# Optimization experiments

Hardware: AMD Instinct MI355X
Metric: run time of the kernel (lower is better)

The kernel has to match this reference:

```python
import jax, jax.numpy as jnp
import numpy as np

D_MODEL = 1024
NUM_HEADS = 16
DEPTH = D_MODEL // NUM_HEADS
MAX_LEN = 5000


def _make_pe(d_model=D_MODEL, max_len=MAX_LEN):
    # Faithful to torch PositionalEncoding: pe shape [max_len, 1, d_model]
    position = np.arange(max_len, dtype=np.float32)[:, None]
    div_term = np.exp(np.arange(0, d_model, 2, dtype=np.float32) * (-np.log(10000.0) / d_model))
    pe = np.zeros((max_len, d_model), dtype=np.float32)
    pe[:, 0::2] = np.sin(position * div_term)
    pe[:, 1::2] = np.cos(position * div_term)
    return jnp.asarray(pe[:, None, :])  # [max_len, 1, d_model]


def setup_inputs() -> dict:
    key = jax.random.key(0)
    ks = jax.random.split(key, 11)
    B, S, D = 4, 2048, D_MODEL
    s = 1.0 / np.sqrt(D)
    inp = {
        "v": jax.random.normal(ks[0], (B, S, D), jnp.float32),
        "k": jax.random.normal(ks[1], (B, S, D), jnp.float32),
        "q": jax.random.normal(ks[2], (B, S, D), jnp.float32),
        "wq_w": jax.random.normal(ks[3], (D, D), jnp.float32) * s,
        "wq_b": jnp.zeros((D,), jnp.float32),
        "wk_w": jax.random.normal(ks[4], (D, D), jnp.float32) * s,
        "wk_b": jnp.zeros((D,), jnp.float32),
        "wv_w": jax.random.normal(ks[5], (D, D), jnp.float32) * s,
        "wv_b": jnp.zeros((D,), jnp.float32),
        "dense_w": jax.random.normal(ks[6], (D, D), jnp.float32) * s,
        "dense_b": jnp.zeros((D,), jnp.float32),
        "pe": _make_pe(),
    }
    return inp


def _split_heads(x, B):
    # [B, S, D] -> [B, H, S, depth]
    return x.reshape(B, -1, NUM_HEADS, DEPTH).transpose(0, 2, 1, 3)


def reference(v, k, q, wq_w, wq_b, wk_w, wk_b, wv_w, wv_b, dense_w, dense_b, pe):
    B = q.shape[0]
    # Faithful bug-reproduction: pe[:batch] has shape [B, 1, D], broadcast over seq.
    pe_b = pe[:B]  # [B, 1, D]
    q = q + pe_b
    k = k + pe_b
    v = v + pe_b
    # Linear layers (torch: x @ W.T + b)
    qh = _split_heads(q @ wq_w.T + wq_b, B)  # [B,H,Sq,d]
    kh = _split_heads(k @ wk_w.T + wk_b, B)  # [B,H,Sk,d]
    vh = _split_heads(v @ wv_w.T + wv_b, B)  # [B,H,Sk,d]
    scale = 1.0 / jnp.sqrt(jnp.float32(DEPTH))
    logits = jnp.einsum("bhqd,bhkd->bhqk", qh, kh) * scale
    attn = jax.nn.softmax(logits, axis=-1)
    out = jnp.einsum("bhqk,bhkd->bhqd", attn, vh)
    out = out.transpose(0, 2, 1, 3).reshape(B, -1, D_MODEL)
    return out @ dense_w.T + dense_b
```

## Files before the change

kernel.cpp:

```cpp
#include <hip/hip_runtime.h>
#include <hip/hip_bf16.h>

typedef short short8 __attribute__((ext_vector_type(8)));
typedef float f32x4 __attribute__((ext_vector_type(4)));
typedef float f32x16 __attribute__((ext_vector_type(16)));
typedef unsigned int uint4v __attribute__((ext_vector_type(4)));

#define MFMA16(a, b, c) __builtin_amdgcn_mfma_f32_16x16x32_bf16(a, b, c, 0, 0, 0)
#define MFMA32(a, b, c) __builtin_amdgcn_mfma_f32_32x32x16_bf16(a, b, c, 0, 0, 0)

typedef __attribute__((address_space(1))) const unsigned int gas_u32;
typedef __attribute__((address_space(3))) unsigned int las_u32;

__device__ inline void gll16(const void* g, void* l) {
    __builtin_amdgcn_global_load_lds((gas_u32*)g, (las_u32*)l, 16, 0, 0);
}

__device__ inline unsigned short f2bf(float f) {
    unsigned u = __builtin_bit_cast(unsigned, f);
    u += 0x7fff + ((u >> 16) & 1);
    return (unsigned short)(u >> 16);
}

__device__ inline unsigned pk_trunc(float a, float b) {
    unsigned ua = __builtin_bit_cast(unsigned, a);
    unsigned ub = __builtin_bit_cast(unsigned, b);
    return (ua >> 16) | (ub & 0xFFFF0000u);
}

__device__ inline float exp2_fast(float x) {
#if __has_builtin(__builtin_amdgcn_exp2f)
    return __builtin_amdgcn_exp2f(x);
#else
    float r; asm("v_exp_f32 %0, %1" : "=v"(r) : "v"(x)); return r;
#endif
}

__device__ inline void pl32_swap(unsigned &a, unsigned &b) {
    asm volatile("v_permlane32_swap_b32 %0, %1" : "+v"(a), "+v"(b));
}

__global__ void pe_cast3(const float* __restrict__ q, const float* __restrict__ k,
                         const float* __restrict__ v, const float* __restrict__ pe,
                         unsigned short* __restrict__ oq, unsigned short* __restrict__ ok,
                         unsigned short* __restrict__ ov) {
    const float* x = (blockIdx.y == 0) ? q : (blockIdx.y == 1) ? k : v;
    unsigned short* o = (blockIdx.y == 0) ? oq : (blockIdx.y == 1) ? ok : ov;
    int i = blockIdx.x * 256 + threadIdx.x;
    long e = (long)i * 4;
    int b = (int)(e >> 21);
    int d = (int)(e & 1023);
    float4 xv = reinterpret_cast<const float4*>(x)[i];
    float4 pv = *reinterpret_cast<const float4*>(pe + b * 1024 + d);
    ushort4 r;
    r.x = f2bf(xv.x + pv.x); r.y = f2bf(xv.y + pv.y);
    r.z = f2bf(xv.z + pv.z); r.w = f2bf(xv.w + pv.w);
    reinterpret_cast<ushort4*>(o)[i] = r;
}

__global__ void wcast4(const float* __restrict__ w0, const float* __restrict__ w1,
                       const float* __restrict__ w2, const float* __restrict__ w3,
                       unsigned short* __restrict__ o0) {
    const float* w = (blockIdx.y == 0) ? w0 : (blockIdx.y == 1) ? w1
                   : (blockIdx.y == 2) ? w2 : w3;
    unsigned short* o = o0 + (size_t)blockIdx.y * 1024 * 1024;
    int i = blockIdx.x * 256 + threadIdx.x;
    float4 xv = reinterpret_cast<const float4*>(w)[i];
    ushort4 r;
    r.x = f2bf(xv.x); r.y = f2bf(xv.y); r.z = f2bf(xv.z); r.w = f2bf(xv.w);
    reinterpret_cast<ushort4*>(o)[i] = r;
}

template <int MODE>
__global__ __launch_bounds__(256, 4) void gemm3(const unsigned short* __restrict__ A0,
                                                const unsigned short* __restrict__ W0,
                                                const float* __restrict__ bq,
                                                const float* __restrict__ bk,
                                                const float* __restrict__ bv,
                                                void* __restrict__ oq,
                                                void* __restrict__ ok,
                                                void* __restrict__ ov,
                                                float qscale) {
    const int NT = 32;
    __shared__ unsigned short lsA[2][128 * 32];
    __shared__ unsigned short lsB[2][128 * 32];

    int z = (MODE == 3) ? blockIdx.z : 0;
    const unsigned short* A = A0 + (size_t)z * 8192 * 1024;
    const unsigned short* W = W0 + (size_t)z * 1024 * 1024;
    const float* bias = (MODE == 3) ? ((z == 0) ? bq : (z == 1) ? bk : bv) : bq;
    float scale = (MODE == 3 && z == 0) ? qscale : 1.0f;

    int tid = threadIdx.x;
    int wave = tid >> 6, lane = tid & 63, lg = lane >> 4, l15 = lane & 15;
    int brow = blockIdx.x * 128;
    int bcol = blockIdx.y * 128;
    int wr = wave >> 1, wc = wave & 1;

    f32x4 zero4 = {0.f, 0.f, 0.f, 0.f};
    f32x4 acc[4][4];
#pragma unroll
    for (int m = 0; m < 4; ++m)
#pragma unroll
        for (int n = 0; n < 4; ++n) acc[m][n] = zero4;

#define STG(k0, bi) do {                                                        \
        _Pragma("unroll")                                                       \
        for (int j = 0; j < 2; ++j) {                                           \
            int c = j * 256 + wave * 64 + lane;                                 \
            gll16(A + ((long)(brow + (c >> 2)) * 1024 + (k0) + (c & 3) * 8),    \
                  (char*)lsA[bi] + (j * 256 + wave * 64) * 16);                 \
            gll16(W + ((long)(bcol + (c >> 2)) * 1024 + (k0) + (c & 3) * 8),    \
                  (char*)lsB[bi] + (j * 256 + wave * 64) * 16);                 \
        }                                                                       \
    } while (0)

    STG(0, 0);
    __syncthreads();

    int cur = 0;
    for (int t = 0; t < NT; ++t) {
        if (t < NT - 1) STG((t + 1) * 32, cur ^ 1);

        const char* KA = (const char*)lsA[cur];
        const char* KB = (const char*)lsB[cur];
        short8 af[4], bf_[4];
#pragma unroll
        for (int m = 0; m < 4; ++m) {
            int row = wr * 64 + m * 16 + l15;
            af[m] = *(const short8*)(KA + row * 64 + lg * 16);
        }
#pragma unroll
        for (int n = 0; n < 4; ++n) {
            int col = wc * 64 + n * 16 + l15;
            bf_[n] = *(const short8*)(KB + col * 64 + lg * 16);
        }
#pragma unroll
        for (int m = 0; m < 4; ++m)
#pragma unroll
            for (int n = 0; n < 4; ++n) acc[m][n] = MFMA16(af[m], bf_[n], acc[m][n]);

        __syncthreads();
        cur ^= 1;
    }
#undef STG

    void* out = (MODE == 3) ? ((z == 0) ? oq : (z == 1) ? ok : ov) : oq;
#pragma unroll
    for (int m = 0; m < 4; ++m)
#pragma unroll
        for (int n = 0; n < 4; ++n) {
            int col = bcol + wc * 64 + n * 16 + l15;
            float bv_ = bias[col];
#pragma unroll
            for (int r = 0; r < 4; ++r) {
                int row = brow + wr * 64 + m * 16 + lg * 4 + r;
                float v = (acc[m][n][r] + bv_) * scale;
                if (MODE == 1) {
                    ((float*)out)[(long)row * 1024 + col] = v;
                } else {
                    int b = row >> 11, s = row & 2047;
                    if (z < 2) {
                        int h = col >> 6, d = col & 63;
                        ((unsigned short*)out)[(((long)(b * 16 + h) * 2048 + s) * 64 + d)] = f2bf(v);
                    } else {
                        ((unsigned short*)out)[((long)(b * 1024 + col)) * 2048 + s] = f2bf(v);
                    }
                }
            }
        }
}

__global__ __launch_bounds__(256, 2) void attn_kernel(const unsigned short* __restrict__ Qh,
                                                      const unsigned short* __restrict__ Kh,
                                                      const unsigned short* __restrict__ Vt,
                                                      unsigned short* __restrict__ Om) {
    const int S = 2048;
    const int NT = S / 64;
    int flat = blockIdx.x;
    int nf_ = (flat & 7) * 64 + (flat >> 3);
    int qt = nf_ & 7;
    int bh = nf_ >> 3;
    int b = bh >> 4, h = bh & 15;

    int tid = threadIdx.x, wave = tid >> 6, lane = tid & 63;
    int l31 = lane & 31, hi = lane >> 5;

    __shared__ __align__(16) unsigned short Kl[3][4096];
    __shared__ __align__(16) unsigned short Vtl[3][4096];

    const unsigned short* Qb = Qh + (long)bh * S * 64;
    const unsigned short* Kb = Kh + (long)bh * S * 64;
    const unsigned short* Vb = Vt + (long)bh * 64 * S;

    int colS = ((((tid & 7) * 16) ^ (((tid >> 3) & 7) << 4)) >> 1);
    const unsigned short* srcK = Kb + (tid >> 3) * 64 + colS;
    const unsigned short* srcV = Vb + (tid >> 3) * 2048 + colS;

    short8 aq[2][4];
    {
        const unsigned short* qrow = Qb + (long)(qt * 256 + wave * 64 + l31) * 64 + hi * 8;
#pragma unroll
        for (int qf = 0; qf < 2; ++qf)
#pragma unroll
            for (int s = 0; s < 4; ++s)
                aq[qf][s] = *(const short8*)(qrow + qf * 32 * 64 + s * 16);
    }

    f32x16 oacc[2][2], lacc[2];
#pragma unroll
    for (int r = 0; r < 16; ++r) {
        oacc[0][0][r] = 0.f; oacc[0][1][r] = 0.f;
        oacc[1][0][r] = 0.f; oacc[1][1][r] = 0.f;
        lacc[0][r] = 0.f; lacc[1][r] = 0.f;
    }

    const short8 ones8 = {0x3F80, 0x3F80, 0x3F80, 0x3F80, 0x3F80, 0x3F80, 0x3F80, 0x3F80};

    int rb0 = l31 * 128;
    int swz = (l31 & 7) << 4;

#define STAGE(kt, bi) do {                                              \
        const unsigned short* sk = srcK + (kt) * 4096;                  \
        gll16(sk,         (char*)Kl[bi] + wave * 1024);                 \
        gll16(sk + 2048,  (char*)Kl[bi] + 4096 + wave * 1024);          \
        const unsigned short* sv = srcV + (kt) * 64;                    \
        gll16(sv,         (char*)Vtl[bi] + wave * 1024);                \
        gll16(sv + 65536, (char*)Vtl[bi] + 4096 + wave * 1024);         \
    } while (0)

    STAGE(0, 0);
    STAGE(1, 1);

    int bi = 0, sb = 2;
    for (int kt = 0; kt < NT; ++kt) {
        if (kt == NT - 1) { asm volatile("s_waitcnt vmcnt(0)" ::: "memory"); }
        else              { asm volatile("s_waitcnt vmcnt(4)" ::: "memory"); }
        __builtin_amdgcn_s_barrier();
        if (kt < NT - 2) STAGE(kt + 2, sb);

        const char* KlC = (const char*)Kl[bi];
        const char* VlC = (const char*)Vtl[bi];

        f32x16 sacc[2][2];
#pragma unroll
        for (int r = 0; r < 16; ++r) {
            sacc[0][0][r] = 0.f; sacc[0][1][r] = 0.f;
            sacc[1][0][r] = 0.f; sacc[1][1][r] = 0.f;
        }
#pragma unroll
        for (int blk = 0; blk < 2; ++blk)
#pragma unroll
            for (int s = 0; s < 4; ++s) {
                short8 kf = *(const short8*)(KlC + blk * 4096 + rb0 + ((32 * s + 16 * hi) ^ swz));
                sacc[0][blk] = MFMA32(kf, aq[0][s], sacc[0][blk]);
                sacc[1][blk] = MFMA32(kf, aq[1][s], sacc[1][blk]);
            }

#pragma unroll
        for (int qf = 0; qf < 2; ++qf)
#pragma unroll
            for (int blk = 0; blk < 2; ++blk)
#pragma unroll
                for (int r = 0; r < 16; ++r) sacc[qf][blk][r] = exp2_fast(sacc[qf][blk][r]);

#pragma unroll
        for (int s = 0; s < 4; ++s) {
            const int blk = s >> 1, base = (s & 1) * 8;
            short8 pa[2];
#pragma unroll
            for (int qf = 0; qf < 2; ++qf) {
                unsigned q0 = pk_trunc(sacc[qf][blk][base + 0], sacc[qf][blk][base + 1]);
                unsigned q1 = pk_trunc(sacc[qf][blk][base + 2], sacc[qf][blk][base + 3]);
                unsigned q2 = pk_trunc(sacc[qf][blk][base + 4], sacc[qf][blk][base + 5]);
                unsigned q3 = pk_trunc(sacc[qf][blk][base + 6], sacc[qf][blk][base + 7]);
                pl32_swap(q0, q2);
                pl32_swap(q1, q3);
                uint4v pw; pw[0] = q0; pw[1] = q1; pw[2] = q2; pw[3] = q3;
                pa[qf] = __builtin_bit_cast(short8, pw);
            }
#pragma unroll
            for (int dblk = 0; dblk < 2; ++dblk) {
                short8 vf = *(const short8*)(VlC + dblk * 4096 + rb0 + ((32 * s + 16 * hi) ^ swz));
                oacc[0][dblk] = MFMA32(pa[0], vf, oacc[0][dblk]);
                oacc[1][dblk] = MFMA32(pa[1], vf, oacc[1][dblk]);
            }
            lacc[0] = MFMA32(pa[0], ones8, lacc[0]);
            lacc[1] = MFMA32(pa[1], ones8, lacc[1]);
        }
        bi = (bi == 2) ? 0 : bi + 1;
        sb = (sb == 2) ? 0 : sb + 1;
    }
#undef STAGE

#pragma unroll
    for (int qf = 0; qf < 2; ++qf) {
        float inv[16];
#pragma unroll
        for (int r = 0; r < 16; ++r) inv[r] = 1.0f / lacc[qf][r];
        int qrow0 = qt * 256 + wave * 64 + qf * 32 + 4 * hi;
#pragma unroll
        for (int dblk = 0; dblk < 2; ++dblk)
#pragma unroll
            for (int r = 0; r < 16; ++r) {
                int qrow = qrow0 + (r & 3) + 8 * (r >> 2);
                int d = h * 64 + dblk * 32 + l31;
                float v = oacc[qf][dblk][r] * inv[r];
                Om[((long)b * 2048 + qrow) * 1024 + d] = f2bf(v);
            }
    }
}

extern "C" void kernel_launch(void* const* d_in, const int* in_sizes, int n_in,
                              void* d_out, int out_size, void* d_ws, size_t ws_size,
                              hipStream_t stream) {
    const float* v_in = (const float*)d_in[0];
    const float* k_in = (const float*)d_in[1];
    const float* q_in = (const float*)d_in[2];
    const float* wq_w = (const float*)d_in[3];
    const float* wq_b = (const float*)d_in[4];
    const float* wk_w = (const float*)d_in[5];
    const float* wk_b = (const float*)d_in[6];
    const float* wv_w = (const float*)d_in[7];
    const float* wv_b = (const float*)d_in[8];
    const float* wd_w = (const float*)d_in[9];
    const float* wd_b = (const float*)d_in[10];
    const float* pe   = (const float*)d_in[11];

    const long SZ = 8192L * 1024 * 2;
    char* ws = (char*)d_ws;
    unsigned short* xq = (unsigned short*)(ws + 0);
    unsigned short* xk = (unsigned short*)(ws + SZ);
    unsigned short* xv = (unsigned short*)(ws + 2 * SZ);
    unsigned short* qh = (unsigned short*)(ws + 3 * SZ);
    unsigned short* kh = (unsigned short*)(ws + 4 * SZ);
    unsigned short* vt = (unsigned short*)(ws + 5 * SZ);
    unsigned short* wqb16 = (unsigned short*)(ws + 6 * SZ);

    pe_cast3<<<dim3(8192, 3), 256, 0, stream>>>(q_in, k_in, v_in, pe, xq, xk, xv);
    wcast4<<<dim3(1024, 4), 256, 0, stream>>>(wq_w, wk_w, wv_w, wd_w, wqb16);

    const float QSCALE = 0.125f * 1.44269504088896f;
    gemm3<3><<<dim3(64, 8, 3), 256, 0, stream>>>(
        xq, wqb16, wq_b, wk_b, wv_b, qh, kh, vt, QSCALE);

    unsigned short* om = xq;
    attn_kernel<<<512, 256, 0, stream>>>(qh, kh, vt, om);

    gemm3<1><<<dim3(64, 8, 1), 256, 0, stream>>>(
        om, wqb16 + 3L * 1024 * 1024, wd_b, nullptr, nullptr, d_out, nullptr, nullptr, 1.0f);
}
```

Before: 221.8 us.

## Triple-buffer projection GEMM with swizzled LDS, add MFMA priority hints

The projection GEMM moves from double to triple buffering. Loads are issued two tiles ahead and the loop waits with vmcnt plus a single barrier per iteration, replacing two __syncthreads. The LDS layout gets an XOR swizzle on both the write and read side to cut bank conflicts, and the occupancy hint drops from 4 to 3 blocks to make room for the extra LDS. The attention kernel seeds its first MFMA from a zero register instead of zeroing the accumulators each tile, packs bf16 pairs with v_perm_b32, and wraps the MFMA sections in s_setprio.

```diff
diff --git a/kernel.cpp b/kernel.cpp
--- a/kernel.cpp
+++ b/kernel.cpp
@@ -22,10 +22,12 @@
     return (unsigned short)(u >> 16);
 }
 
-__device__ inline unsigned pk_trunc(float a, float b) {
-    unsigned ua = __builtin_bit_cast(unsigned, a);
-    unsigned ub = __builtin_bit_cast(unsigned, b);
-    return (ua >> 16) | (ub & 0xFFFF0000u);
+__device__ inline unsigned pk_perm(float a, float b, unsigned sel) {
+    unsigned r;
+    asm("v_perm_b32 %0, %1, %2, %3"
+        : "=v"(r)
+        : "v"(__builtin_bit_cast(unsigned, b)), "v"(__builtin_bit_cast(unsigned, a)), "s"(sel));
+    return r;
 }
 
 __device__ inline float exp2_fast(float x) {
@@ -72,7 +74,7 @@
 }
 
 template <int MODE>
-__global__ __launch_bounds__(256, 4) void gemm3(const unsigned short* __restrict__ A0,
+__global__ __launch_bounds__(256, 3) void gemm3(const unsigned short* __restrict__ A0,
                                                 const unsigned short* __restrict__ W0,
                                                 const float* __restrict__ bq,
                                                 const float* __restrict__ bk,
@@ -82,8 +84,8 @@
                                                 void* __restrict__ ov,
                                                 float qscale) {
     const int NT = 32;
-    __shared__ unsigned short lsA[2][128 * 32];
-    __shared__ unsigned short lsB[2][128 * 32];
+    __shared__ unsigned short lsA[3][128 * 32];
+    __shared__ unsigned short lsB[3][128 * 32];
 
     int z = (MODE == 3) ? blockIdx.z : 0;
     const unsigned short* A = A0 + (size_t)z * 8192 * 1024;
@@ -97,6 +99,14 @@
     int bcol = blockIdx.y * 128;
     int wr = wave >> 1, wc = wave & 1;
 
+    int c0 = wave * 64 + lane, c1 = 256 + c0;
+    const unsigned short* sA0 = A + (long)(brow + (c0 >> 2)) * 1024 + ((c0 ^ (c0 >> 2)) & 3) * 8;
+    const unsigned short* sA1 = A + (long)(brow + (c1 >> 2)) * 1024 + ((c1 ^ (c1 >> 2)) & 3) * 8;
+    const unsigned short* sB0 = W + (long)(bcol + (c0 >> 2)) * 1024 + ((c0 ^ (c0 >> 2)) & 3) * 8;
+    const unsigned short* sB1 = W + (long)(bcol + (c1 >> 2)) * 1024 + ((c1 ^ (c1 >> 2)) & 3) * 8;
+
+    int cread = (lg * 16) ^ ((l15 & 3) << 4);
+
     f32x4 zero4 = {0.f, 0.f, 0.f, 0.f};
     f32x4 acc[4][4];
 #pragma unroll
@@ -104,44 +114,45 @@
 #pragma unroll
         for (int n = 0; n < 4; ++n) acc[m][n] = zero4;
 
-#define STG(k0, bi) do {                                                        \
-        _Pragma("unroll")                                                       \
-        for (int j = 0; j < 2; ++j) {                                           \
-            int c = j * 256 + wave * 64 + lane;                                 \
-            gll16(A + ((long)(brow + (c >> 2)) * 1024 + (k0) + (c & 3) * 8),    \
-                  (char*)lsA[bi] + (j * 256 + wave * 64) * 16);                 \
-            gll16(W + ((long)(bcol + (c >> 2)) * 1024 + (k0) + (c & 3) * 8),    \
-                  (char*)lsB[bi] + (j * 256 + wave * 64) * 16);                 \
-        }                                                                       \
+#define STG(k0, bi) do {                                                  \
+        gll16(sA0 + (k0), (char*)lsA[bi] + (wave * 64) * 16);             \
+        gll16(sA1 + (k0), (char*)lsA[bi] + (256 + wave * 64) * 16);       \
+        gll16(sB0 + (k0), (char*)lsB[bi] + (wave * 64) * 16);             \
+        gll16(sB1 + (k0), (char*)lsB[bi] + (256 + wave * 64) * 16);       \
     } while (0)
 
     STG(0, 0);
-    __syncthreads();
-
-    int cur = 0;
+    STG(32, 1);
+
+    int bi = 0, sb = 2;
     for (int t = 0; t < NT; ++t) {
-        if (t < NT - 1) STG((t + 1) * 32, cur ^ 1);
-
-        const char* KA = (const char*)lsA[cur];
-        const char* KB = (const char*)lsB[cur];
+        if (t == NT - 1) { asm volatile("s_waitcnt vmcnt(0)" ::: "memory"); }
+        else             { asm volatile("s_waitcnt vmcnt(4)" ::: "memory"); }
+        __builtin_amdgcn_s_barrier();
+        if (t < NT - 2) STG((t + 2) * 32, sb);
+
+        const char* KA = (const char*)lsA[bi];
+        const char* KB = (const char*)lsB[bi];
         short8 af[4], bf_[4];
 #pragma unroll
         for (int m = 0; m < 4; ++m) {
             int row = wr * 64 + m * 16 + l15;
-            af[m] = *(const short8*)(KA + row * 64 + lg * 16);
+            af[m] = *(const short8*)(KA + row * 64 + cread);
         }
 #pragma unroll
         for (int n = 0; n < 4; ++n) {
             int col = wc * 64 + n * 16 + l15;
-            bf_[n] = *(const short8*)(KB + col * 64 + lg * 16);
-        }
+            bf_[n] = *(const short8*)(KB + col * 64 + cread);
+        }
+        __builtin_amdgcn_s_setprio(1);
 #pragma unroll
         for (int m = 0; m < 4; ++m)
 #pragma unroll
             for (int n = 0; n < 4; ++n) acc[m][n] = MFMA16(af[m], bf_[n], acc[m][n]);
-
-        __syncthreads();
-        cur ^= 1;
+        __builtin_amdgcn_s_setprio(0);
+
+        bi = (bi == 2) ? 0 : bi + 1;
+        sb = (sb == 2) ? 0 : sb + 1;
     }
 #undef STG
 
@@ -207,15 +218,17 @@
                 aq[qf][s] = *(const short8*)(qrow + qf * 32 * 64 + s * 16);
     }
 
-    f32x16 oacc[2][2], lacc[2];
+    f32x16 oacc[2][2], lacc[2], z16;
 #pragma unroll
     for (int r = 0; r < 16; ++r) {
         oacc[0][0][r] = 0.f; oacc[0][1][r] = 0.f;
         oacc[1][0][r] = 0.f; oacc[1][1][r] = 0.f;
         lacc[0][r] = 0.f; lacc[1][r] = 0.f;
+        z16[r] = 0.f;
     }
 
     const short8 ones8 = {0x3F80, 0x3F80, 0x3F80, 0x3F80, 0x3F80, 0x3F80, 0x3F80, 0x3F80};
+    const unsigned SEL = 0x07060302u;
 
     int rb0 = l31 * 128;
     int swz = (l31 & 7) << 4;
@@ -243,19 +256,20 @@
         const char* VlC = (const char*)Vtl[bi];
 
         f32x16 sacc[2][2];
-#pragma unroll
-        for (int r = 0; r < 16; ++r) {
-            sacc[0][0][r] = 0.f; sacc[0][1][r] = 0.f;
-            sacc[1][0][r] = 0.f; sacc[1][1][r] = 0.f;
-        }
-#pragma unroll
-        for (int blk = 0; blk < 2; ++blk)
-#pragma unroll
-            for (int s = 0; s < 4; ++s) {
+        __builtin_amdgcn_s_setprio(1);
+#pragma unroll
+        for (int blk = 0; blk < 2; ++blk) {
+            short8 kf0 = *(const short8*)(KlC + blk * 4096 + rb0 + ((16 * hi) ^ swz));
+            sacc[0][blk] = MFMA32(kf0, aq[0][0], z16);
+            sacc[1][blk] = MFMA32(kf0, aq[1][0], z16);
+#pragma unroll
+            for (int s = 1; s < 4; ++s) {
                 short8 kf = *(const short8*)(KlC + blk * 4096 + rb0 + ((32 * s + 16 * hi) ^ swz));
                 sacc[0][blk] = MFMA32(kf, aq[0][s], sacc[0][blk]);
                 sacc[1][blk] = MFMA32(kf, aq[1][s], sacc[1][blk]);
             }
+        }
+        __builtin_amdgcn_s_setprio(0);
 
 #pragma unroll
         for (int qf = 0; qf < 2; ++qf)
@@ -270,15 +284,16 @@
             short8 pa[2];
 #pragma unroll
             for (int qf = 0; qf < 2; ++qf) {
-                unsigned q0 = pk_trunc(sacc[qf][blk][base + 0], sacc[qf][blk][base + 1]);
-                unsigned q1 = pk_trunc(sacc[qf][blk][base + 2], sacc[qf][blk][base + 3]);
-                unsigned q2 = pk_trunc(sacc[qf][blk][base + 4], sacc[qf][blk][base + 5]);
-                unsigned q3 = pk_trunc(sacc[qf][blk][base + 6], sacc[qf][blk][base + 7]);
+                unsigned q0 = pk_perm(sacc[qf][blk][base + 0], sacc[qf][blk][base + 1], SEL);
+                unsigned q1 = pk_perm(sacc[qf][blk][base + 2], sacc[qf][blk][base + 3], SEL);
+                unsigned q2 = pk_perm(sacc[qf][blk][base + 4], sacc[qf][blk][base + 5], SEL);
+                unsigned q3 = pk_perm(sacc[qf][blk][base + 6], sacc[qf][blk][base + 7], SEL);
                 pl32_swap(q0, q2);
                 pl32_swap(q1, q3);
                 uint4v pw; pw[0] = q0; pw[1] = q1; pw[2] = q2; pw[3] = q3;
                 pa[qf] = __builtin_bit_cast(short8, pw);
             }
+            __builtin_amdgcn_s_setprio(1);
 #pragma unroll
             for (int dblk = 0; dblk < 2; ++dblk) {
                 short8 vf = *(const short8*)(VlC + dblk * 4096 + rb0 + ((32 * s + 16 * hi) ^ swz));
@@ -287,6 +302,7 @@
             }
             lacc[0] = MFMA32(pa[0], ones8, lacc[0]);
             lacc[1] = MFMA32(pa[1], ones8, lacc[1]);
+            __builtin_amdgcn_s_setprio(0);
         }
         bi = (bi == 2) ? 0 : bi + 1;
         sb = (sb == 2) ? 0 : sb + 1;
```

Result: no change. 217.5 us (-1.9%).
